# Kernel tuning notes

Hardware: AMD Instinct MI355X
Metric: run time of the kernel (lower is better)

## Reference

```python
import jax, jax.numpy as jnp
import numpy as np

NU, NT, E, H = 100000, 200000, 1000000, 64
NUM_LAYERS = 3


def setup_inputs() -> dict:
    key = jax.random.key(0)
    ks = jax.random.split(key, 16)
    s = 0.05
    inp = {}
    inp["x_user"] = jax.random.normal(ks[0], (NU, 32), jnp.float32)
    inp["x_transaction"] = jax.random.normal(ks[1], (NT, 64), jnp.float32)
    inp["ei_u2u"] = jax.random.randint(ks[2], (2, E), 0, NU, jnp.int32)
    inp["ei_t2t"] = jax.random.randint(ks[3], (2, E), 0, NT, jnp.int32)
    inp["ei_u2t"] = jnp.stack([jax.random.randint(ks[4], (E,), 0, NU),
                               jax.random.randint(ks[5], (E,), 0, NT)]).astype(jnp.int32)
    inp["ei_t2u"] = jnp.stack([jax.random.randint(ks[6], (E,), 0, NT),
                               jax.random.randint(ks[7], (E,), 0, NU)]).astype(jnp.int32)
    inp["W_emb_user"] = jax.random.normal(ks[8], (32, H), jnp.float32) * s
    inp["b_emb_user"] = jnp.zeros((H,), jnp.float32)
    inp["W_emb_txn"] = jax.random.normal(ks[9], (64, H), jnp.float32) * s
    inp["b_emb_txn"] = jnp.zeros((H,), jnp.float32)
    # one GCNConv weight/bias per (layer, edge_type): order u2u, t2t, u2t, t2u
    inp["conv_W"] = jax.random.normal(ks[10], (NUM_LAYERS, 4, H, H), jnp.float32) * s
    inp["conv_b"] = jnp.zeros((NUM_LAYERS, 4, H), jnp.float32)
    inp["W1"] = jax.random.normal(ks[11], (H, H), jnp.float32) * s
    inp["b1"] = jnp.zeros((H,), jnp.float32)
    inp["W2"] = jax.random.normal(ks[12], (H, 1), jnp.float32) * s
    inp["b2"] = jnp.zeros((1,), jnp.float32)
    return inp


def _gcn(h_src, ei, n_src, n_dst, W, b, self_loops):
    """GCNConv: x W with symmetric degree normalization, scatter-sum into dst."""
    src, dst = ei[0], ei[1]
    if self_loops:  # same node type on both ends: add self loops (PyG default)
        loop = jnp.arange(n_dst, dtype=src.dtype)
        src = jnp.concatenate([src, loop])
        dst = jnp.concatenate([dst, loop])
        deg = jax.ops.segment_sum(jnp.ones_like(dst, jnp.float32), dst, num_segments=n_dst)
        dinv = jnp.where(deg > 0, jax.lax.rsqrt(jnp.maximum(deg, 1.0)), 0.0)
        norm = dinv[src] * dinv[dst]
    else:  # bipartite relation: out-degree of src, in-degree of dst
        ds = jax.ops.segment_sum(jnp.ones_like(src, jnp.float32), src, num_segments=n_src)
        dd = jax.ops.segment_sum(jnp.ones_like(dst, jnp.float32), dst, num_segments=n_dst)
        dsi = jnp.where(ds > 0, jax.lax.rsqrt(jnp.maximum(ds, 1.0)), 0.0)
        ddi = jnp.where(dd > 0, jax.lax.rsqrt(jnp.maximum(dd, 1.0)), 0.0)
        norm = dsi[src] * ddi[dst]
    m = h_src @ W  # [N_src, H] transform first (GCNConv order)
    out = jax.ops.segment_sum(m[src] * norm[:, None], dst, num_segments=n_dst)
    return out + b


def reference(x_user, x_transaction, ei_u2u, ei_t2t, ei_u2t, ei_t2u,
              W_emb_user, b_emb_user, W_emb_txn, b_emb_txn,
              conv_W, conv_b, W1, b1, W2, b2):
    hu = x_user @ W_emb_user + b_emb_user          # [NU, H]
    ht = x_transaction @ W_emb_txn + b_emb_txn     # [NT, H]
    for l in range(NUM_LAYERS):
        ou1 = _gcn(hu, ei_u2u, NU, NU, conv_W[l, 0], conv_b[l, 0], True)
        ot1 = _gcn(ht, ei_t2t, NT, NT, conv_W[l, 1], conv_b[l, 1], True)
        ot2 = _gcn(hu, ei_u2t, NU, NT, conv_W[l, 2], conv_b[l, 2], False)
        ou2 = _gcn(ht, ei_t2u, NT, NU, conv_W[l, 3], conv_b[l, 3], False)
        # HeteroConv aggr='mean' across relations per dst type, then ReLU
        hu = jax.nn.relu((ou1 + ou2) * 0.5)
        ht = jax.nn.relu((ot1 + ot2) * 0.5)
    g = jnp.stack([hu.mean(axis=0), ht.mean(axis=0)])  # [2, H] per-type global mean
    x = g.mean(axis=0, keepdims=True)                  # [1, H]
    x = jax.nn.relu(x @ W1 + b1)                       # dropout is identity at eval
    return jax.nn.sigmoid(x @ W2 + b2)                 # [1, 1]
```

## Files before the change

kernel.cpp:

```cpp
#include <hip/hip_runtime.h>
#include <hip/hip_bf16.h>
#include <hip/hip_fp8.h>

#define NU_ 100000
#define NT_ 200000
#define NE_ 1000000
#define HD  64
#define NL  3

#define OFF0 0
#define OFF1 (NU_)
#define OFF4 (2 * NU_ + 2 * NT_)
#define OFF5 (3 * NU_ + 2 * NT_)
#define HTOT (3 * NU_ + 3 * NT_)
#define RPT2 (NU_ + NT_)

#define PB1  512
#define BKP  2048
#define NBKC 147
#define NBKS 147
#define NBKT (NBKC + NBKS)

#define WPK_EMBU 0
#define WPK_EMBT 2048
#define WPK_CONV 6144
#define WPK_G0U  55296
#define WPK_G0T  59392
#define WPK_TOT  67584
#define PK_ELEMS (WPK_TOT + 256)
#define PKB      ((PK_ELEMS + 255) / 256)

#define GMU 512
#define GMT 1024
#define GBU 3125
#define GBT 6250

typedef float floatx2 __attribute__((ext_vector_type(2)));
typedef _Float16 f16x8 __attribute__((ext_vector_type(8)));
typedef float f32x4 __attribute__((ext_vector_type(4)));
typedef unsigned short u16x8 __attribute__((ext_vector_type(8)));

__device__ __forceinline__ unsigned char enc_fp8(float v) {
    return (unsigned char)__hip_cvt_float_to_fp8(v, __HIP_SATFINITE, __HIP_E4M3);
}

__device__ __forceinline__ float dec1_fp8(unsigned int u) {
    int e = (u >> 3) & 15;
    int m = u & 7;
    int mant = m | (e ? 8 : 0);
    if (u & 0x80) mant = -mant;
    int ex = (e ? e : 1) - 10;
    return (float)mant * __uint_as_float((unsigned int)(ex + 127) << 23);
}

__device__ __forceinline__ void dec4_fp8(unsigned int u, float* f) {
#if __has_builtin(__builtin_amdgcn_cvt_pk_f32_fp8)
    floatx2 lo = __builtin_amdgcn_cvt_pk_f32_fp8((int)u, false);
    floatx2 hi = __builtin_amdgcn_cvt_pk_f32_fp8((int)u, true);
    f[0] = lo.x; f[1] = lo.y; f[2] = hi.x; f[3] = hi.y;
#else
    f[0] = dec1_fp8(u & 0xff);
    f[1] = dec1_fp8((u >> 8) & 0xff);
    f[2] = dec1_fp8((u >> 16) & 0xff);
    f[3] = dec1_fp8((u >> 24) & 0xff);
#endif
}

__global__ void detect_dtype(const unsigned short* __restrict__ x, int* __restrict__ flag, int n) {
    __shared__ int s_big;
    if (threadIdx.x == 0) s_big = 0;
    __syncthreads();
    int big = 0;
    for (int i = threadIdx.x; i < n; i += blockDim.x) {
        float v = __uint_as_float(((unsigned int)x[i]) << 16);
        if (!(fabsf(v) < 1.0e4f)) big = 1;
    }
    if (big) atomicAdd(&s_big, 1);
    __syncthreads();
    if (threadIdx.x == 0) flag[0] = (s_big > 0) ? 0 : 1;
}

struct Ptr10 { const void* p[10]; };

__global__ void cvt_weights(Ptr10 src, float* __restrict__ dst, float* __restrict__ gsum,
                            int* __restrict__ gcnt, const int* __restrict__ flag) {
    const int c[11] = {0, 2048, 2112, 6208, 6272, 55424, 56192, 60288, 60352, 60416, 60417};
    int i = blockIdx.x * blockDim.x + threadIdx.x;
    if (i < 64) gsum[i] = 0.f;
    if (i < NBKT) gcnt[i] = 0;
    if (i >= 60417) return;
    int r = 0;
#pragma unroll
    for (int k = 1; k < 10; ++k)
        if (i >= c[k]) r = k;
    int e = i - c[r];
    if (flag[0]) {
        unsigned short u = ((const unsigned short*)src.p[r])[e];
        dst[i] = __uint_as_float(((unsigned int)u) << 16);
    } else {
        dst[i] = ((const float*)src.p[r])[e];
    }
}

__device__ __forceinline__ void pack_dev(int gid, const float* __restrict__ wts,
                                         _Float16* __restrict__ wpk,
                                         float* __restrict__ bcomp) {
    if (gid >= PK_ELEMS) return;
    if (gid < WPK_G0U) {
        const float* W;
        int r, KS;
        if (gid < WPK_EMBT) { W = wts; r = gid; KS = 1; }
        else if (gid < WPK_CONV) { W = wts + 2112; r = gid - WPK_EMBT; KS = 2; }
        else {
            int mat = (gid - WPK_CONV) >> 12;
            W = wts + 6272 + mat * 4096;
            r = (gid - WPK_CONV) & 4095;
            KS = 2;
        }
        int j = r & 7;
        int lane = (r >> 3) & 63;
        int f = r >> 9;
        int ct = f / KS;
        int s = f - ct * KS;
        int k = 32 * s + 8 * (lane >> 4) + j;
        int n = 16 * ct + (lane & 15);
        wpk[gid] = (_Float16)W[k * 64 + n];
    } else if (gid < WPK_TOT) {
        const float* We;
        int matc, rr, KS;
        if (gid < WPK_G0T) {
            int r = gid - WPK_G0U;
            matc = (r >> 11) ? 2 : 0;
            rr = r & 2047;
            We = wts;
            KS = 1;
        } else {
            int r = gid - WPK_G0T;
            matc = (r >> 12) ? 3 : 1;
            rr = r & 4095;
            We = wts + 2112;
            KS = 2;
        }
        const float* Wc = wts + 6272 + matc * 4096;
        int j = rr & 7;
        int lane = (rr >> 3) & 63;
        int f = rr >> 9;
        int ct = f / KS;
        int s = f - ct * KS;
        int k = 32 * s + 8 * (lane >> 4) + j;
        int n = 16 * ct + (lane & 15);
        float acc = 0.f;
#pragma unroll
        for (int q = 0; q < 64; ++q)
            acc = fmaf(We[k * 64 + q], Wc[q * 64 + n], acc);
        wpk[gid] = (_Float16)acc;
    } else {
        int q = gid - WPK_TOT;
        int mat = q >> 6;
        int n = q & 63;
        const float* be = (mat == 0 || mat == 2) ? (wts + 2048) : (wts + 6208);
        const float* Wc = wts + 6272 + mat * 4096;
        float acc = 0.f;
#pragma unroll
        for (int k = 0; k < 64; ++k)
            acc = fmaf(be[k], Wc[k * 64 + n], acc);
        bcomp[q] = acc;
    }
}

__device__ __forceinline__ void p1_dev(int bid, const int* __restrict__ eu2u,
                                       const int* __restrict__ et2t,
                                       const int* __restrict__ eu2t,
                                       const int* __restrict__ et2u,
                                       int* __restrict__ gcnt, int* __restrict__ bofs) {
    __shared__ int cnt[NBKT];
    for (int j = threadIdx.x; j < NBKT; j += 256) cnt[j] = 0;
    __syncthreads();
    for (int i = bid * 256 + threadIdx.x; i < 6 * NE_; i += PB1 * 256) {
        int b;
        if (i < 4 * NE_) {
            int m;
            if (i < NE_)          m = eu2u[i + NE_];
            else if (i < 2 * NE_) m = NU_ + et2t[i];
            else if (i < 3 * NE_) m = NU_ + eu2t[i - NE_];
            else                  m = et2u[i - 2 * NE_];
            b = m >> 11;
        } else {
            int m2 = (i < 5 * NE_) ? eu2t[i - 4 * NE_] : (NU_ + et2u[i - 5 * NE_]);
            b = NBKC + (m2 >> 11);
        }
        atomicAdd(&cnt[b], 1);
    }
    __syncthreads();
    for (int j = threadIdx.x; j < NBKT; j += 256) {
        bofs[bid * NBKT + j] = atomicAdd(&gcnt[j], cnt[j]);
    }
}

__global__ __launch_bounds__(256) void fused_p1_pack(
    const int* __restrict__ eu2u, const int* __restrict__ et2t,
    const int* __restrict__ eu2t, const int* __restrict__ et2u,
    int* __restrict__ gcnt, int* __restrict__ bofs,
    const float* __restrict__ wts, _Float16* __restrict__ wpk, float* __restrict__ bcomp) {
    int b = blockIdx.x;
    if (b < PB1) {
        p1_dev(b, eu2u, et2t, eu2t, et2u, gcnt, bofs);
    } else {
        pack_dev((b - PB1) * 256 + threadIdx.x, wts, wpk, bcomp);
    }
}

__global__ __launch_bounds__(256) void p2_scatter(
    const int* __restrict__ eu2u, const int* __restrict__ et2t,
    const int* __restrict__ eu2t, const int* __restrict__ et2u,
    const int* __restrict__ gcnt, int* __restrict__ gbase, const int* __restrict__ bofs,
    unsigned int* __restrict__ part_csr, unsigned int* __restrict__ part_src) {
    __shared__ int gb[NBKT];
    __shared__ int lofs[NBKT];
    const int t = threadIdx.x;
    for (int j = t; j < NBKT; j += 256) { lofs[j] = 0; gb[j] = gcnt[j]; }
    __syncthreads();
    if (t == 0) {
        int s = 0;
        for (int j = 0; j < NBKC; ++j) { int c = gb[j]; gb[j] = s; s += c; }
        s = 0;
        for (int j = NBKC; j < NBKT; ++j) { int c = gb[j]; gb[j] = s; s += c; }
    }
    __syncthreads();
    const int bid = blockIdx.x;
    if (bid == 0)
        for (int j = t; j < NBKT; j += 256) gbase[j] = gb[j];
    for (int i = bid * 256 + t; i < 6 * NE_; i += PB1 * 256) {
        if (i < 4 * NE_) {
            int m; unsigned int src, tag;
            if (i < NE_)          { m = eu2u[i + NE_];        src = (unsigned int)eu2u[i];           tag = 0u; }
            else if (i < 2 * NE_) { m = NU_ + et2t[i];        src = (unsigned int)et2t[i - NE_];     tag = 0u; }
            else if (i < 3 * NE_) { m = NU_ + eu2t[i - NE_];  src = (unsigned int)eu2t[i - 2 * NE_]; tag = 1u; }
            else                  { m = et2u[i - 2 * NE_];    src = (unsigned int)et2u[i - 3 * NE_]; tag = 1u; }
            int b = m >> 11;
            int l = atomicAdd(&lofs[b], 1);
            int pos = gb[b] + bofs[bid * NBKT + b] + l;
            part_csr[pos] = (src << 12) | (tag << 11) | (unsigned int)(m & (BKP - 1));
        } else {
            int m2 = (i < 5 * NE_) ? eu2t[i - 4 * NE_] : (NU_ + et2u[i - 5 * NE_]);
            int b = NBKC + (m2 >> 11);
            int l = atomicAdd(&lofs[b], 1);
            int pos = gb[b] + bofs[bid * NBKT + b] + l;
            part_src[pos] = (unsigned int)m2;
        }
    }
}

__global__ __launch_bounds__(1024) void bucket_build(
    const unsigned int* __restrict__ part_csr, const unsigned int* __restrict__ part_src,
    const int* __restrict__ gcnt, const int* __restrict__ gbase,
    float* __restrict__ dinv, int4* __restrict__ meta,
    int* __restrict__ colU, int* __restrict__ colT) {
    const int b = blockIdx.x;
    const int t = threadIdx.x;
    if (b >= NBKC) {
        __shared__ int cS[BKP];
        const int n = gcnt[b];
        const int base = gbase[b];
        for (int j = t; j < BKP; j += 1024) cS[j] = 0;
        __syncthreads();
        for (int i = t; i < n; i += 1024)
            atomicAdd(&cS[(int)(part_src[base + i] & (BKP - 1))], 1);
        __syncthreads();
        const int m0 = (b - NBKC) << 11;
        for (int j = t; j < BKP; j += 1024) {
            int m2 = m0 + j;
            if (m2 < NU_ + NT_) {
                int o = (m2 < NU_) ? (OFF4 + m2) : (OFF5 + (m2 - NU_));
                int h = cS[j];
                dinv[o] = (h > 0) ? rsqrtf((float)h) : 0.f;
            }
        }
        return;
    }
    __shared__ int cA[BKP];
    __shared__ int cB[BKP];
    __shared__ int lp[BKP];
    __shared__ int s1[1024];
    const int n = gcnt[b];
    const int base = gbase[b];
    for (int j = t; j < BKP; j += 1024) { cA[j] = 0; cB[j] = 0; }
    __syncthreads();
    for (int i = t; i < n; i += 1024) {
        unsigned int it = part_csr[base + i];
        int l = (int)(it & (BKP - 1));
        if (it & 0x800u) atomicAdd(&cB[l], 1);
        else             atomicAdd(&cA[l], 1);
    }
    __syncthreads();
    const int j0 = t << 1, j1 = j0 + 1;
    const int a0 = cA[j0] + cB[j0];
    const int a1 = cA[j1] + cB[j1];
    const int ps = a0 + a1;
    s1[t] = ps;
    __syncthreads();
    for (int off = 1; off < 1024; off <<= 1) {
        int x = (t >= off) ? s1[t - off] : 0;
        __syncthreads();
        s1[t] += x;
        __syncthreads();
    }
    const int excl = s1[t] - ps;
    lp[j0] = excl;
    lp[j1] = excl + a0;
    __syncthreads();
    const int m0 = b << 11;
    const int gb0 = gbase[b];
    for (int j = t; j < BKP; j += 1024) {
        int m = m0 + j;
        if (m < NU_ + NT_) {
            int hA = cA[j], hB = cB[j];
            float dslf = rsqrtf((float)hA + 1.0f);
            int oA = (m < NU_) ? (OFF0 + m) : (OFF1 + (m - NU_));
            dinv[oA] = dslf;
            int4 mt;
            mt.x = gb0 + lp[j] - ((m >= NU_) ? 2 * NE_ : 0);
            mt.y = hA + hB;
            mt.z = __float_as_int(0.5f * dslf);
            mt.w = __float_as_int((hB > 0) ? 0.5f * rsqrtf((float)hB) : 0.f);
            meta[m] = mt;
        }
    }
    __syncthreads();
    for (int j = t; j < BKP; j += 1024) cA[j] = 0;
    __syncthreads();
    for (int i = t; i < n; i += 1024) {
        unsigned int it = part_csr[base + i];
        int mlow = (int)(it & (BKP - 1));
        int ofs = atomicAdd(&cA[mlow], 1);
        int g = gb0 + lp[mlow] + ofs;
        int colv = (int)(((it >> 12) << 6) | ((it & 0x800u) << 20));
        int m = m0 + mlow;
        if (m < NU_) colU[g] = colv;
        else         colT[g - 2 * NE_] = colv;
    }
}

template <int K>
__device__ __forceinline__ void gemm0_dev(int t0, int tstride, int ntiles,
                                          const void* __restrict__ x,
                                          const _Float16* __restrict__ WApk,
                                          const _Float16* __restrict__ WBpk,
                                          const float* __restrict__ bA,
                                          const float* __restrict__ bB,
                                          const float* __restrict__ scA,
                                          const float* __restrict__ scB,
                                          unsigned char* __restrict__ mA,
                                          unsigned char* __restrict__ mB,
                                          const int* __restrict__ flag) {
    constexpr int KS = K / 32;
    const int lane = threadIdx.x & 63;
    const int rq = lane & 15;
    const int oct = lane >> 4;

    f16x8 bf[2][4][KS];
#pragma unroll
    for (int m = 0; m < 2; ++m) {
        const _Float16* P = m ? WBpk : WApk;
#pragma unroll
        for (int ct = 0; ct < 4; ++ct)
#pragma unroll
            for (int s = 0; s < KS; ++s)
                bf[m][ct][s] = *(const f16x8*)(P + (((ct * KS + s) << 9) + (lane << 3)));
    }
    float bvA[4], bvB[4];
#pragma unroll
    for (int ct = 0; ct < 4; ++ct) { bvA[ct] = bA[16 * ct + rq]; bvB[ct] = bB[16 * ct + rq]; }

    const bool isb = flag[0] != 0;

    for (int t = t0; t < ntiles; t += tstride) {
        const int r0 = t << 4;
        f16x8 a[KS];
        if (isb) {
            const unsigned short* xr = (const unsigned short*)x + (size_t)(r0 + rq) * K + 8 * oct;
#pragma unroll
            for (int s = 0; s < KS; ++s) {
                u16x8 uv = *(const u16x8*)(xr + 32 * s);
                f16x8 v;
#pragma unroll
                for (int j = 0; j < 8; ++j)
                    v[j] = (_Float16)__uint_as_float(((unsigned int)uv[j]) << 16);
                a[s] = v;
            }
        } else {
            const float* xr = (const float*)x + (size_t)(r0 + rq) * K + 8 * oct;
#pragma unroll
            for (int s = 0; s < KS; ++s) {
                float4 x0 = *(const float4*)(xr + 32 * s);
                float4 x1 = *(const float4*)(xr + 32 * s + 4);
                f16x8 v;
                v[0] = (_Float16)x0.x; v[1] = (_Float16)x0.y;
                v[2] = (_Float16)x0.z; v[3] = (_Float16)x0.w;
                v[4] = (_Float16)x1.x; v[5] = (_Float16)x1.y;
                v[6] = (_Float16)x1.z; v[7] = (_Float16)x1.w;
                a[s] = v;
            }
        }

        f32x4 acc[2][4];
#pragma unroll
        for (int m = 0; m < 2; ++m)
#pragma unroll
            for (int ct = 0; ct < 4; ++ct) acc[m][ct] = (f32x4){0.f, 0.f, 0.f, 0.f};
#pragma unroll
        for (int m = 0; m < 2; ++m)
#pragma unroll
            for (int ct = 0; ct < 4; ++ct)
#pragma unroll
                for (int s = 0; s < KS; ++s)
                    acc[m][ct] = __builtin_amdgcn_mfma_f32_16x16x32_f16(a[s], bf[m][ct][s],
                                                                       acc[m][ct], 0, 0, 0);

        const int rb = r0 + (oct << 2);
        float sa[4], sb[4];
#pragma unroll
        for (int g = 0; g < 4; ++g) { sa[g] = scA[rb + g]; sb[g] = scB[rb + g]; }
#pragma unroll
        for (int ct = 0; ct < 4; ++ct)
#pragma unroll
            for (int g = 0; g < 4; ++g) {
                mA[(size_t)(rb + g) * HD + 16 * ct + rq] =
                    enc_fp8((acc[0][ct][g] + bvA[ct]) * sa[g]);
                mB[(size_t)(rb + g) * HD + 16 * ct + rq] =
                    enc_fp8((acc[1][ct][g] + bvB[ct]) * sb[g]);
            }
    }
}

__global__ __launch_bounds__(256) void gemm0_both(
    const void* __restrict__ x_user, const void* __restrict__ x_txn,
    const _Float16* __restrict__ wpk, const float* __restrict__ bcomp,
    const float* __restrict__ dinv,
    unsigned char* __restrict__ m_uu, unsigned char* __restrict__ m_ut,
    unsigned char* __restrict__ m_tt, unsigned char* __restrict__ m_tu,
    const int* __restrict__ flag) {
    int b = blockIdx.x;
    int wid = threadIdx.x >> 6;
    if (b < GMU) {
        gemm0_dev<32>(b * 4 + wid, GMU * 4, NU_ / 16, x_user,
                      wpk + WPK_G0U, wpk + WPK_G0U + 2048,
                      bcomp + 0, bcomp + 128,
                      dinv + OFF0, dinv + OFF4, m_uu, m_ut, flag);
    } else {
        gemm0_dev<64>((b - GMU) * 4 + wid, GMT * 4, NT_ / 16, x_txn,
                      wpk + WPK_G0T, wpk + WPK_G0T + 4096,
                      bcomp + 64, bcomp + 192,
                      dinv + OFF1, dinv + OFF5, m_tt, m_tu, flag);
    }
}

__device__ __forceinline__ void gather_phase(int d, bool valid,
                                             const unsigned char* __restrict__ msg,
                                             unsigned int offB,
                                             const int4* __restrict__ meta,
                                             const int* __restrict__ col,
                                             const float* __restrict__ ba,
                                             const float* __restrict__ bb,
                                             float* __restrict__ af) {
    const int lane = threadIdx.x & 63;
    const int grp = lane >> 3;
    const int sub = lane & 7;

    int4 mt = make_int4(0, 0, 0, 0);
    if (valid) mt = meta[d];
    const int st = mt.x;
    const int cnt = mt.y;
    const float dA = __int_as_float(mt.z);
    const float dB = __int_as_float(mt.w);
    const unsigned char* msgL = msg + (sub << 3);

    floatx2 acc[4];
#pragma unroll
    for (int q = 0; q < 4; ++q) acc[q] = (floatx2){0.f, 0.f};

    auto consume = [&](uint2 u, float s) {
        floatx2 s2; s2.x = s; s2.y = s;
#if __has_builtin(__builtin_amdgcn_cvt_pk_f32_fp8)
        acc[0] += __builtin_amdgcn_cvt_pk_f32_fp8((int)u.x, false) * s2;
        acc[1] += __builtin_amdgcn_cvt_pk_f32_fp8((int)u.x, true) * s2;
        acc[2] += __builtin_amdgcn_cvt_pk_f32_fp8((int)u.y, false) * s2;
        acc[3] += __builtin_amdgcn_cvt_pk_f32_fp8((int)u.y, true) * s2;
#else
        float f[8];
        dec4_fp8(u.x, f);
        dec4_fp8(u.y, f + 4);
        acc[0].x += f[0] * s; acc[0].y += f[1] * s;
        acc[1].x += f[2] * s; acc[1].y += f[3] * s;
        acc[2].x += f[4] * s; acc[2].y += f[5] * s;
        acc[3].x += f[6] * s; acc[3].y += f[7] * s;
#endif
    };

    if (valid) {
        uint2 uself = *(const uint2*)(msgL + ((unsigned int)d << 6));
        consume(uself, dA);
    }

    int cw = (sub < cnt) ? col[st + sub] : 0;
    int done = 0;
    while (done < cnt) {
        int rem = cnt - done;
        if (rem > 8) rem = 8;

        uint2 ub0, ub1, ub2, ub3, ub4, ub5, ub6, ub7;
        float sc0, sc1, sc2, sc3, sc4, sc5, sc6, sc7;

        auto issue = [&](int p, uint2& ub, float& sc) {
            int c = __shfl(cw, (grp << 3) + p);
            unsigned int off = ((unsigned int)c & 0x7fffffffu) + ((c < 0) ? offB : 0u);
            sc = (p < rem) ? ((c < 0) ? dB : dA) : 0.f;
            ub = *(const uint2*)(msgL + off);
        };

        issue(0, ub0, sc0);
        issue(1, ub1, sc1);
        issue(2, ub2, sc2);
        issue(3, ub3, sc3);
        issue(4, ub4, sc4);
        issue(5, ub5, sc5);
        issue(6, ub6, sc6);
        issue(7, ub7, sc7);

        int nd = done + 8;
        int cw2 = (nd + sub < cnt) ? col[st + nd + sub] : 0;

        consume(ub0, sc0);
        consume(ub1, sc1);
        consume(ub2, sc2);
        consume(ub3, sc3);
        consume(ub4, sc4);
        consume(ub5, sc5);
        consume(ub6, sc6);
        consume(ub7, sc7);

        cw = cw2;
        done = nd;
    }

    const int col0 = sub << 3;
    float4 a0 = *(const float4*)(ba + col0);
    float4 a1 = *(const float4*)(ba + col0 + 4);
    float4 c0 = *(const float4*)(bb + col0);
    float4 c1 = *(const float4*)(bb + col0 + 4);
    float av[8] = {acc[0].x, acc[0].y, acc[1].x, acc[1].y,
                   acc[2].x, acc[2].y, acc[3].x, acc[3].y};
    float bv[8] = {a0.x + c0.x, a0.y + c0.y, a0.z + c0.z, a0.w + c0.w,
                   a1.x + c1.x, a1.y + c1.y, a1.z + c1.z, a1.w + c1.w};
#pragma unroll
    for (int k = 0; k < 8; ++k)
        af[k] = fmaxf(av[k] + 0.5f * bv[k], 0.f);
}

__global__ __launch_bounds__(256) void gather_both(
    const unsigned char* __restrict__ msgU, const unsigned char* __restrict__ msgT,
    const int4* __restrict__ meta,
    const int* __restrict__ colU, const int* __restrict__ colT,
    const float* __restrict__ bU0, const float* __restrict__ bU1,
    const float* __restrict__ bT0, const float* __restrict__ bT1,
    _Float16* __restrict__ hu, _Float16* __restrict__ ht) {
    int b = blockIdx.x;
    const bool isU = b < GBU;
    const int blk = isU ? b : b - GBU;
    const int grp = (threadIdx.x & 63) >> 3;
    const int sub = threadIdx.x & 7;
    const int d = (blk << 5) + ((threadIdx.x >> 6) << 3) + grp;
    const int N = isU ? NU_ : NT_;
    float af[8];
    gather_phase(d, d < N,
                 isU ? msgU : msgT, (unsigned int)(isU ? NU_ : NT_) * HD,
                 isU ? meta : meta + NU_, isU ? colU : colT,
                 isU ? bU0 : bT0, isU ? bU1 : bT1, af);
    if (d < N) {
        _Float16* out = isU ? hu : ht;
        f16x8 o;
#pragma unroll
        for (int k = 0; k < 8; ++k) o[k] = (_Float16)af[k];
        *(f16x8*)(out + ((size_t)d << 6) + (sub << 3)) = o;
    }
}

__global__ __launch_bounds__(256) void gather_gemm_both(
    const unsigned char* __restrict__ msgU, const unsigned char* __restrict__ msgT,
    const int4* __restrict__ meta,
    const int* __restrict__ colU, const int* __restrict__ colT,
    const float* __restrict__ bU0, const float* __restrict__ bU1,
    const float* __restrict__ bT0, const float* __restrict__ bT1,
    const _Float16* __restrict__ WUa, const _Float16* __restrict__ WUb,
    const _Float16* __restrict__ WTa, const _Float16* __restrict__ WTb,
    const float* __restrict__ dinv,
    unsigned char* __restrict__ o_uu, unsigned char* __restrict__ o_ut,
    unsigned char* __restrict__ o_tt, unsigned char* __restrict__ o_tu) {
    __shared__ _Float16 hs[32][64];
    int b = blockIdx.x;
    const bool isU = b < GBU;
    const int blk = isU ? b : b - GBU;
    const int lane = threadIdx.x & 63;
    const int grp = lane >> 3;
    const int sub = lane & 7;
    const int w = threadIdx.x >> 6;
    const int d = (blk << 5) + (w << 3) + grp;
    const int N = isU ? NU_ : NT_;

    float af[8];
    gather_phase(d, d < N,
                 isU ? msgU : msgT, (unsigned int)(isU ? NU_ : NT_) * HD,
                 isU ? meta : meta + NU_, isU ? colU : colT,
                 isU ? bU0 : bT0, isU ? bU1 : bT1, af);

    {
        const int ld = threadIdx.x >> 3;
        f16x8 o;
#pragma unroll
        for (int k = 0; k < 8; ++k) o[k] = (_Float16)af[k];
        *(f16x8*)(&hs[ld][sub << 3]) = o;
    }
    __syncthreads();

    if (w < 2) {
        const _Float16* Pa = isU ? WUa : WTa;
        const _Float16* Pb = isU ? WUb : WTb;
        unsigned char* mA = isU ? o_uu : o_tt;
        unsigned char* mB = isU ? o_ut : o_tu;
        const float* scA = dinv + (isU ? OFF0 : OFF1);
        const float* scB = dinv + (isU ? OFF4 : OFF5);
        const int rq = lane & 15;
        const int oct = lane >> 4;

        f16x8 bf[2][4][2];
#pragma unroll
        for (int m = 0; m < 2; ++m) {
            const _Float16* P = m ? Pb : Pa;
#pragma unroll
            for (int ct = 0; ct < 4; ++ct)
#pragma unroll
                for (int s = 0; s < 2; ++s)
                    bf[m][ct][s] = *(const f16x8*)(P + ((((ct << 1) + s) << 9) + (lane << 3)));
        }

        f16x8 a0 = *(const f16x8*)(&hs[16 * w + rq][8 * oct]);
        f16x8 a1 = *(const f16x8*)(&hs[16 * w + rq][32 + 8 * oct]);

        f32x4 acc[2][4];
#pragma unroll
        for (int m = 0; m < 2; ++m)
#pragma unroll
            for (int ct = 0; ct < 4; ++ct) acc[m][ct] = (f32x4){0.f, 0.f, 0.f, 0.f};
#pragma unroll
        for (int m = 0; m < 2; ++m)
#pragma unroll
            for (int ct = 0; ct < 4; ++ct) {
                acc[m][ct] = __builtin_amdgcn_mfma_f32_16x16x32_f16(a0, bf[m][ct][0],
                                                                   acc[m][ct], 0, 0, 0);
                acc[m][ct] = __builtin_amdgcn_mfma_f32_16x16x32_f16(a1, bf[m][ct][1],
                                                                   acc[m][ct], 0, 0, 0);
            }

        const int rb = (blk << 5) + 16 * w + (oct << 2);
        float sa[4], sb[4];
#pragma unroll
        for (int g = 0; g < 4; ++g) { sa[g] = scA[rb + g]; sb[g] = scB[rb + g]; }
#pragma unroll
        for (int ct = 0; ct < 4; ++ct)
#pragma unroll
            for (int g = 0; g < 4; ++g) {
                mA[(size_t)(rb + g) * HD + 16 * ct + rq] = enc_fp8(acc[0][ct][g] * sa[g]);
                mB[(size_t)(rb + g) * HD + 16 * ct + rq] = enc_fp8(acc[1][ct][g] * sb[g]);
            }
    }
}

__global__ __launch_bounds__(256) void colmean_both(const _Float16* __restrict__ hu,
                                                    const _Float16* __restrict__ ht,
                                                    float* __restrict__ gsum) {
    const bool isU = blockIdx.x < 512;
    const _Float16* h = isU ? hu : ht;
    const int n = isU ? NU_ : NT_;
    const float scale = isU ? 0.5f / NU_ : 0.5f / NT_;
    const int blk = isU ? blockIdx.x : blockIdx.x - 512;
    const int lane = threadIdx.x & 63;
    const int w = threadIdx.x >> 6;
    float s = 0.f;
    for (int r = blk * 4 + w; r < n; r += 512 * 4)
        s += (float)h[(size_t)r * HD + lane];
    __shared__ float red[256];
    red[threadIdx.x] = s;
    __syncthreads();
    if (threadIdx.x < 64) {
        float t = red[threadIdx.x] + red[64 + threadIdx.x] + red[128 + threadIdx.x] +
                  red[192 + threadIdx.x];
        atomicAdd(&gsum[lane], t * scale);
    }
}

__global__ void head(const float* __restrict__ g, const float* __restrict__ W1,
                     const float* __restrict__ b1, const float* __restrict__ W2,
                     const float* __restrict__ b2, const int* __restrict__ flag,
                     void* __restrict__ out) {
    const int c = threadIdx.x;
    float x = b1[c];
    for (int k = 0; k < HD; ++k) x = fmaf(g[k], W1[k * HD + c], x);
    x = fmaxf(x, 0.f);
    float t = x * W2[c];
    for (int off = 32; off; off >>= 1) t += __shfl_down(t, off);
    if (c == 0) {
        float z = t + b2[0];
        float s = 1.f / (1.f + expf(-z));
        if (flag[0]) *(__hip_bfloat16*)out = __float2bfloat16(s);
        else *(float*)out = s;
    }
}

extern "C" void kernel_launch(void* const* d_in, const int* in_sizes, int n_in,
                              void* d_out, int out_size, void* d_ws, size_t ws_size,
                              hipStream_t stream) {
    const void* x_user = d_in[0];
    const void* x_txn  = d_in[1];
    const int* ei_u2u = (const int*)d_in[2];
    const int* ei_t2t = (const int*)d_in[3];
    const int* ei_u2t = (const int*)d_in[4];
    const int* ei_t2u = (const int*)d_in[5];

    float* ws = (float*)d_ws;
    _Float16* hu = (_Float16*)ws;
    _Float16* ht = hu + (size_t)NU_ * HD;
    float* dinv = (float*)(ht + (size_t)NT_ * HD);
    float* wts = dinv + HTOT;
    float* gsum = wts + 60432;
    float* bcomp = gsum + 64;
    _Float16* wpk = (_Float16*)(bcomp + 256);
    unsigned char* msg0 = (unsigned char*)(wpk + WPK_TOT);
    unsigned char* msg1 = msg0 + (size_t)(2 * NU_ + 2 * NT_) * HD;
    int* aux  = (int*)(msg1 + (size_t)(2 * NU_ + 2 * NT_) * HD);
    int* colU = aux + 2 * NBKT + PB1 * NBKT;
    int* colT = colU + 2 * NE_;
    int4* meta = (int4*)(colT + 2 * NE_);
    int* dflag = (int*)(meta + RPT2);

    int* gcnt  = aux;
    int* gbase = gcnt + NBKT;
    int* bofs  = gbase + NBKT;

    auto uu = [](unsigned char* s) { return s; };
    auto tu = [](unsigned char* s) { return s + (size_t)NU_ * HD; };
    auto tt = [](unsigned char* s) { return s + (size_t)(NU_ + NT_) * HD; };
    auto ut = [](unsigned char* s) { return s + (size_t)(NU_ + 2 * NT_) * HD; };

    unsigned int* part_csr = (unsigned int*)msg1;
    unsigned int* part_src = (unsigned int*)hu;

    float* W1f = wts + 56192;
    float* b1f = W1f + 4096;
    float* W2f = b1f + 64;
    float* b2f = W2f + 64;
    const float* convbf = wts + 55424;

    detect_dtype<<<1, 256, 0, stream>>>((const unsigned short*)x_user, dflag, 2048);
    {
        Ptr10 p;
        for (int k = 0; k < 10; ++k) p.p[k] = d_in[6 + k];
        cvt_weights<<<(60417 + 255) / 256, 256, 0, stream>>>(p, wts, gsum, gcnt, dflag);
    }

    fused_p1_pack<<<PB1 + PKB, 256, 0, stream>>>(ei_u2u, ei_t2t, ei_u2t, ei_t2u,
                                                 gcnt, bofs, wts, wpk, bcomp);

    p2_scatter<<<PB1, 256, 0, stream>>>(ei_u2u, ei_t2t, ei_u2t, ei_t2u,
                                        gcnt, gbase, bofs, part_csr, part_src);

    bucket_build<<<NBKT, 1024, 0, stream>>>(part_csr, part_src, gcnt, gbase,
                                            dinv, meta, colU, colT);

    gemm0_both<<<GMU + GMT, 256, 0, stream>>>(x_user, x_txn, wpk, bcomp, dinv,
                                              uu(msg0), ut(msg0), tt(msg0), tu(msg0), dflag);

    for (int l = 0; l < 2; ++l) {
        unsigned char* in  = (l == 0) ? msg0 : msg1;
        unsigned char* out = (l == 0) ? msg1 : msg0;
        const float* B0   = convbf + ((size_t)l * 4 + 0) * HD;
        const float* Bt   = convbf + ((size_t)l * 4 + 1) * HD;
        const float* Bu2t = convbf + ((size_t)l * 4 + 2) * HD;
        const float* Bt2u = convbf + ((size_t)l * 4 + 3) * HD;
        const _Float16* W0n   = wpk + WPK_CONV + ((size_t)(l + 1) * 4 + 0) * 4096;
        const _Float16* Wtn   = wpk + WPK_CONV + ((size_t)(l + 1) * 4 + 1) * 4096;
        const _Float16* Wu2tn = wpk + WPK_CONV + ((size_t)(l + 1) * 4 + 2) * 4096;
        const _Float16* Wt2un = wpk + WPK_CONV + ((size_t)(l + 1) * 4 + 3) * 4096;

        gather_gemm_both<<<GBU + GBT, 256, 0, stream>>>(
            uu(in), tt(in), meta, colU, colT,
            B0, Bt2u, Bt, Bu2t,
            W0n, Wu2tn, Wtn, Wt2un, dinv,
            uu(out), ut(out), tt(out), tu(out));
    }

    {
        const float* B0   = convbf + (2 * 4 + 0) * HD;
        const float* Bt   = convbf + (2 * 4 + 1) * HD;
        const float* Bu2t = convbf + (2 * 4 + 2) * HD;
        const float* Bt2u = convbf + (2 * 4 + 3) * HD;
        gather_both<<<GBU + GBT, 256, 0, stream>>>(uu(msg0), tt(msg0),
                                                   meta, colU, colT,
                                                   B0, Bt2u, Bt, Bu2t, hu, ht);
    }

    colmean_both<<<1024, 256, 0, stream>>>(hu, ht, gsum);
    head<<<1, 64, 0, stream>>>(gsum, W1f, b1f, W2f, b2f, dflag, d_out);
}
```

Measured before the change: 552.8 us.

## Fuse final-layer column reduction into gather and split MFMA work across all waves

The last gather kernel now reduces its 32 rows per block into per-block column partial sums in shared memory instead of writing full fp16 hu/ht tensors. A small kernel then sums those partials, replacing the colmean pass that reread 300k rows. Separately, the gather+GEMM kernel spreads its two weight products across all four waves, one matrix per wave pair, instead of having two waves do both. Together these remove a large intermediate write and reread and idle waves, at the cost of extra block syncs and per-block partial buffers.

```diff
diff --git a/kernel.cpp b/kernel.cpp
--- a/kernel.cpp
+++ b/kernel.cpp
@@ -557,31 +557,44 @@
         af[k] = fmaxf(av[k] + 0.5f * bv[k], 0.f);
 }
 
-__global__ __launch_bounds__(256) void gather_both(
+__global__ __launch_bounds__(256) void gather_red_both(
     const unsigned char* __restrict__ msgU, const unsigned char* __restrict__ msgT,
     const int4* __restrict__ meta,
     const int* __restrict__ colU, const int* __restrict__ colT,
     const float* __restrict__ bU0, const float* __restrict__ bU1,
     const float* __restrict__ bT0, const float* __restrict__ bT1,
-    _Float16* __restrict__ hu, _Float16* __restrict__ ht) {
+    float* __restrict__ partU, float* __restrict__ partT) {
+    __shared__ float hs[32][64];
+    __shared__ float ps[4][64];
     int b = blockIdx.x;
     const bool isU = b < GBU;
     const int blk = isU ? b : b - GBU;
     const int grp = (threadIdx.x & 63) >> 3;
     const int sub = threadIdx.x & 7;
-    const int d = (blk << 5) + ((threadIdx.x >> 6) << 3) + grp;
+    const int w = threadIdx.x >> 6;
+    const int d = (blk << 5) + (w << 3) + grp;
     const int N = isU ? NU_ : NT_;
     float af[8];
     gather_phase(d, d < N,
                  isU ? msgU : msgT, (unsigned int)(isU ? NU_ : NT_) * HD,
                  isU ? meta : meta + NU_, isU ? colU : colT,
                  isU ? bU0 : bT0, isU ? bU1 : bT1, af);
-    if (d < N) {
-        _Float16* out = isU ? hu : ht;
-        f16x8 o;
-#pragma unroll
-        for (int k = 0; k < 8; ++k) o[k] = (_Float16)af[k];
-        *(f16x8*)(out + ((size_t)d << 6) + (sub << 3)) = o;
+    {
+        const int ld = threadIdx.x >> 3;
+#pragma unroll
+        for (int k = 0; k < 8; ++k) hs[ld][(sub << 3) + k] = (d < N) ? af[k] : 0.f;
+    }
+    __syncthreads();
+    const int c = threadIdx.x & 63;
+    const int r0 = w << 3;
+    float s = 0.f;
+#pragma unroll
+    for (int r = 0; r < 8; ++r) s += hs[r0 + r][c];
+    ps[w][c] = s;
+    __syncthreads();
+    if (threadIdx.x < 64) {
+        float t = ps[0][c] + ps[1][c] + ps[2][c] + ps[3][c];
+        (isU ? partU : partT)[(size_t)blk * 64 + c] = t;
     }
 }
 
@@ -622,72 +635,59 @@
     }
     __syncthreads();
 
-    if (w < 2) {
-        const _Float16* Pa = isU ? WUa : WTa;
-        const _Float16* Pb = isU ? WUb : WTb;
-        unsigned char* mA = isU ? o_uu : o_tt;
-        unsigned char* mB = isU ? o_ut : o_tu;
-        const float* scA = dinv + (isU ? OFF0 : OFF1);
-        const float* scB = dinv + (isU ? OFF4 : OFF5);
+    {
+        const int half = w & 1;
+        const int mi = w >> 1;
+        const _Float16* P = mi ? (isU ? WUb : WTb) : (isU ? WUa : WTa);
+        unsigned char* mOut = mi ? (isU ? o_ut : o_tu) : (isU ? o_uu : o_tt);
+        const float* sc = dinv + (mi ? (isU ? OFF4 : OFF5) : (isU ? OFF0 : OFF1));
         const int rq = lane & 15;
         const int oct = lane >> 4;
 
-        f16x8 bf[2][4][2];
-#pragma unroll
-        for (int m = 0; m < 2; ++m) {
-            const _Float16* P = m ? Pb : Pa;
-#pragma unroll
-            for (int ct = 0; ct < 4; ++ct)
-#pragma unroll
-                for (int s = 0; s < 2; ++s)
-                    bf[m][ct][s] = *(const f16x8*)(P + ((((ct << 1) + s) << 9) + (lane << 3)));
+        f16x8 bf[4][2];
+#pragma unroll
+        for (int ct = 0; ct < 4; ++ct)
+#pragma unroll
+            for (int s = 0; s < 2; ++s)
+                bf[ct][s] = *(const f16x8*)(P + ((((ct << 1) + s) << 9) + (lane << 3)));
+
+        f16x8 a0 = *(const f16x8*)(&hs[16 * half + rq][8 * oct]);
+        f16x8 a1 = *(const f16x8*)(&hs[16 * half + rq][32 + 8 * oct]);
+
+        f32x4 acc[4];
+#pragma unroll
+        for (int ct = 0; ct < 4; ++ct) acc[ct] = (f32x4){0.f, 0.f, 0.f, 0.f};
+#pragma unroll
+        for (int ct = 0; ct < 4; ++ct) {
+            acc[ct] = __builtin_amdgcn_mfma_f32_16x16x32_f16(a0, bf[ct][0], acc[ct], 0, 0, 0);
+            acc[ct] = __builtin_amdgcn_mfma_f32_16x16x32_f16(a1, bf[ct][1], acc[ct], 0, 0, 0);
         }
 
-        f16x8 a0 = *(const f16x8*)(&hs[16 * w + rq][8 * oct]);
-        f16x8 a1 = *(const f16x8*)(&hs[16 * w + rq][32 + 8 * oct]);
-
-        f32x4 acc[2][4];
-#pragma unroll
-        for (int m = 0; m < 2; ++m)
-#pragma unroll
-            for (int ct = 0; ct < 4; ++ct) acc[m][ct] = (f32x4){0.f, 0.f, 0.f, 0.f};
-#pragma unroll
-        for (int m = 0; m < 2; ++m)
-#pragma unroll
-            for (int ct = 0; ct < 4; ++ct) {
-                acc[m][ct] = __builtin_amdgcn_mfma_f32_16x16x32_f16(a0, bf[m][ct][0],
-                                                                   acc[m][ct], 0, 0, 0);
-                acc[m][ct] = __builtin_amdgcn_mfma_f32_16x16x32_f16(a1, bf[m][ct][1],
-                                                                   acc[m][ct], 0, 0, 0);
-            }
-
-        const int rb = (blk << 5) + 16 * w + (oct << 2);
-        float sa[4], sb[4];
-#pragma unroll
-        for (int g = 0; g < 4; ++g) { sa[g] = scA[rb + g]; sb[g] = scB[rb + g]; }
+        const int rb = (blk << 5) + 16 * half + (oct << 2);
+        float sv[4];
+#pragma unroll
+        for (int g = 0; g < 4; ++g) sv[g] = sc[rb + g];
 #pragma unroll
         for (int ct = 0; ct < 4; ++ct)
 #pragma unroll
-            for (int g = 0; g < 4; ++g) {
-                mA[(size_t)(rb + g) * HD + 16 * ct + rq] = enc_fp8(acc[0][ct][g] * sa[g]);
-                mB[(size_t)(rb + g) * HD + 16 * ct + rq] = enc_fp8(acc[1][ct][g] * sb[g]);
-            }
-    }
-}
-
-__global__ __launch_bounds__(256) void colmean_both(const _Float16* __restrict__ hu,
-                                                    const _Float16* __restrict__ ht,
-                                                    float* __restrict__ gsum) {
-    const bool isU = blockIdx.x < 512;
-    const _Float16* h = isU ? hu : ht;
-    const int n = isU ? NU_ : NT_;
+            for (int g = 0; g < 4; ++g)
+                mOut[(size_t)(rb + g) * HD + 16 * ct + rq] = enc_fp8(acc[ct][g] * sv[g]);
+    }
+}
+
+__global__ __launch_bounds__(256) void colmean_small(const float* __restrict__ partU,
+                                                     const float* __restrict__ partT,
+                                                     float* __restrict__ gsum) {
+    const bool isU = blockIdx.x < 8;
+    const float* p = isU ? partU : partT;
+    const int rows = isU ? GBU : GBT;
     const float scale = isU ? 0.5f / NU_ : 0.5f / NT_;
-    const int blk = isU ? blockIdx.x : blockIdx.x - 512;
+    const int blk = isU ? blockIdx.x : blockIdx.x - 8;
     const int lane = threadIdx.x & 63;
-    const int w = threadIdx.x >> 6;
+    const int wv = threadIdx.x >> 6;
     float s = 0.f;
-    for (int r = blk * 4 + w; r < n; r += 512 * 4)
-        s += (float)h[(size_t)r * HD + lane];
+    for (int r = blk * 4 + wv; r < rows; r += 32)
+        s += p[(size_t)r * 64 + lane];
     __shared__ float red[256];
     red[threadIdx.x] = s;
     __syncthreads();
@@ -727,9 +727,9 @@
     const int* ei_t2u = (const int*)d_in[5];
 
     float* ws = (float*)d_ws;
-    _Float16* hu = (_Float16*)ws;
-    _Float16* ht = hu + (size_t)NU_ * HD;
-    float* dinv = (float*)(ht + (size_t)NT_ * HD);
+    float* partU = ws;
+    float* partT = partU + (size_t)GBU * 64;
+    float* dinv = (float*)((_Float16*)ws + (size_t)RPT2 * HD);
     float* wts = dinv + HTOT;
     float* gsum = wts + 60432;
     float* bcomp = gsum + 64;
@@ -752,7 +752,7 @@
     auto ut = [](unsigned char* s) { return s + (size_t)(NU_ + 2 * NT_) * HD; };
 
     unsigned int* part_csr = (unsigned int*)msg1;
-    unsigned int* part_src = (unsigned int*)hu;
+    unsigned int* part_src = (unsigned int*)ws;
 
     float* W1f = wts + 56192;
     float* b1f = W1f + 4096;
@@ -803,11 +803,11 @@
         const float* Bt   = convbf + (2 * 4 + 1) * HD;
         const float* Bu2t = convbf + (2 * 4 + 2) * HD;
         const float* Bt2u = convbf + (2 * 4 + 3) * HD;
-        gather_both<<<GBU + GBT, 256, 0, stream>>>(uu(msg0), tt(msg0),
-                                                   meta, colU, colT,
-                                                   B0, Bt2u, Bt, Bu2t, hu, ht);
-    }
-
-    colmean_both<<<1024, 256, 0, stream>>>(hu, ht, gsum);
+        gather_red_both<<<GBU + GBT, 256, 0, stream>>>(uu(msg0), tt(msg0),
+                                                       meta, colU, colT,
+                                                       B0, Bt2u, Bt, Bu2t, partU, partT);
+    }
+
+    colmean_small<<<16, 256, 0, stream>>>(partU, partT, gsum);
     head<<<1, 64, 0, stream>>>(gsum, W1f, b1f, W2f, b2f, dflag, d_out);
 }
```

After: 552.3 us. About the same (-0.1%).
